# Kernel optimization log

Hardware: AMD Instinct MI355X
Metric: run time of the kernel (lower is better)

The kernel has to match this reference:

```python
import jax, jax.numpy as jnp
import numpy as np

N_NODES = 50000
N_EDGES = 600000
IN_CH = 128
HID_CH = 128
OUT_CH = 16
N_GRAPHS = 512


def gcn_conv(x, edge_index, W, b, n_nodes):
    """PyG GCNConv: add self-loops, symmetric deg normalization, linear, scatter-add."""
    src = edge_index[0]
    dst = edge_index[1]
    loop = jnp.arange(n_nodes, dtype=edge_index.dtype)
    src = jnp.concatenate([src, loop])  # [E+N]
    dst = jnp.concatenate([dst, loop])
    ones = jnp.ones(src.shape[0], dtype=x.dtype)
    deg = jax.ops.segment_sum(ones, dst, num_segments=n_nodes)  # in-degree incl. self-loop
    dinv = jnp.where(deg > 0, jax.lax.rsqrt(deg), 0.0)
    norm = dinv[src] * dinv[dst]  # [E+N]
    h = x @ W  # [N, out] linear-then-propagate, as in PyG GCNConv
    msg = h[src] * norm[:, None]  # gather + scale
    out = jax.ops.segment_sum(msg, dst, num_segments=n_nodes)
    return out + b


def global_mean_pool(x, batch, num_graphs):
    sums = jax.ops.segment_sum(x, batch, num_segments=num_graphs)
    cnt = jax.ops.segment_sum(jnp.ones(x.shape[0], dtype=x.dtype), batch, num_segments=num_graphs)
    return sums / jnp.maximum(cnt, 1.0)[:, None]


def setup_inputs() -> dict:
    key = jax.random.key(0)
    ks = jax.random.split(key, 8)
    x = jax.random.normal(ks[0], (N_NODES, IN_CH), dtype=jnp.float32)
    edge_index = jax.random.randint(ks[1], (2, N_EDGES), 0, N_NODES, dtype=jnp.int64 if jax.config.jax_enable_x64 else jnp.int32)
    batch = jnp.sort(jax.random.randint(ks[2], (N_NODES,), 0, N_GRAPHS, dtype=edge_index.dtype))
    s1 = 1.0 / np.sqrt(IN_CH)
    s2 = 1.0 / np.sqrt(HID_CH)
    W1 = jax.random.uniform(ks[3], (IN_CH, HID_CH), jnp.float32, -s1, s1)
    b1 = jnp.zeros((HID_CH,), jnp.float32)
    W2 = jax.random.uniform(ks[4], (HID_CH, HID_CH), jnp.float32, -s2, s2)
    b2 = jnp.zeros((HID_CH,), jnp.float32)
    Wfc = jax.random.uniform(ks[5], (HID_CH, OUT_CH), jnp.float32, -s2, s2)
    bfc = jax.random.uniform(ks[6], (OUT_CH,), jnp.float32, -s2, s2)
    return {"x": x, "edge_index": edge_index, "batch": batch,
            "W1": W1, "b1": b1, "W2": W2, "b2": b2, "Wfc": Wfc, "bfc": bfc}


def reference(x, edge_index, batch, W1, b1, W2, b2, Wfc, bfc):
    n = x.shape[0]
    h = jax.nn.relu(gcn_conv(x, edge_index, W1, b1, n))
    # dropout is identity in eval mode (training=False)
    h = jax.nn.relu(gcn_conv(h, edge_index, W2, b2, n))
    g = global_mean_pool(h, batch, N_GRAPHS)  # [G, hidden]
    out = jax.nn.sigmoid(g @ Wfc + bfc)  # [G, out]
    return out
```

## Files before the change

### kernel.cpp

```cpp
#include <hip/hip_runtime.h>
#include <hip/hip_fp16.h>
#include <math.h>

#define NN 50000
#define CH 128
#define NG 512
#define OCH 16
#define CAP 64
#define NBINS 196
#define HB 147

typedef _Float16 half8 __attribute__((ext_vector_type(8)));
typedef float f32x4 __attribute__((ext_vector_type(4)));
typedef float f32x2 __attribute__((ext_vector_type(2)));


__device__ __forceinline__ void unpack_fp8x8(uint2 v, float* o) {
    f32x2 a = __builtin_amdgcn_cvt_pk_f32_fp8((int)v.x, false);
    f32x2 b = __builtin_amdgcn_cvt_pk_f32_fp8((int)v.x, true);
    f32x2 c = __builtin_amdgcn_cvt_pk_f32_fp8((int)v.y, false);
    f32x2 d = __builtin_amdgcn_cvt_pk_f32_fp8((int)v.y, true);
    o[0] = a[0]; o[1] = a[1]; o[2] = b[0]; o[3] = b[1];
    o[4] = c[0]; o[5] = c[1]; o[6] = d[0]; o[7] = d[1];
}

__device__ __forceinline__ unsigned char f32_to_fp8(float v) {
    int r = __builtin_amdgcn_cvt_pk_fp8_f32(v, v, 0, false);
    return (unsigned char)(r & 0xFF);
}


__device__ __forceinline__ void gemm1_body(const float* __restrict__ A, const _Float16* __restrict__ Wt,
                                           unsigned char* __restrict__ C, int n, int blk) {
    int wave = threadIdx.x >> 6;
    int lane = threadIdx.x & 63;
    int base = blk * 64 + wave * 16;
    if (base >= n) return;
    int ma = lane & 15;
    int kb = lane >> 4;

    f32x4 acc[8];
#pragma unroll
    for (int t = 0; t < 8; ++t) acc[t] = (f32x4){0.f, 0.f, 0.f, 0.f};

#pragma unroll
    for (int kk = 0; kk < 4; ++kk) {
        int k0 = kk * 32 + kb * 8;
        const float* ap = A + (size_t)(base + ma) * CH + k0;
        float4 a0 = ((const float4*)ap)[0];
        float4 a1 = ((const float4*)ap)[1];
        half8 af;
        af[0] = (_Float16)a0.x; af[1] = (_Float16)a0.y; af[2] = (_Float16)a0.z; af[3] = (_Float16)a0.w;
        af[4] = (_Float16)a1.x; af[5] = (_Float16)a1.y; af[6] = (_Float16)a1.z; af[7] = (_Float16)a1.w;
#pragma unroll
        for (int tn = 0; tn < 8; ++tn) {
            half8 bf = *(const half8*)(Wt + (size_t)(tn * 16 + ma) * CH + k0);
            acc[tn] = __builtin_amdgcn_mfma_f32_16x16x32_f16(af, bf, acc[tn], 0, 0, 0);
        }
    }

    int r0 = base + kb * 4;
#pragma unroll
    for (int tn = 0; tn < 8; ++tn) {
#pragma unroll
        for (int r = 0; r < 4; ++r) {
            C[(size_t)(r0 + r) * CH + tn * 16 + ma] = f32_to_fp8(acc[tn][r]);
        }
    }
}


__global__ __launch_bounds__(256) void k1_hist_init_gemm1_k(const int* __restrict__ dst, int e, int* __restrict__ tableT,
                                                            const int* __restrict__ batch, int n, int* __restrict__ gstart,
                                                            const float* __restrict__ W1, const float* __restrict__ W2,
                                                            _Float16* __restrict__ Wt1, _Float16* __restrict__ Wt2,
                                                            const float* __restrict__ x, unsigned char* __restrict__ h1,
                                                            int* __restrict__ tickets) {
    if ((int)blockIdx.x < HB) {
        __shared__ int hist[NBINS];
        for (int i = threadIdx.x; i < NBINS; i += 256) hist[i] = 0;
        __syncthreads();
#pragma unroll
        for (int j = 0; j < 4; ++j) {
            int idx = blockIdx.x * 4096 + j * 1024 + threadIdx.x * 4;
            if (idx + 3 < e) {
                int4 d = *(const int4*)&dst[idx];
                atomicAdd(&hist[d.x >> 8], 1);
                atomicAdd(&hist[d.y >> 8], 1);
                atomicAdd(&hist[d.z >> 8], 1);
                atomicAdd(&hist[d.w >> 8], 1);
            } else {
                for (int k = idx; k < e && k < idx + 4; ++k) atomicAdd(&hist[dst[k] >> 8], 1);
            }
        }
        __syncthreads();
        for (int i = threadIdx.x; i < NBINS; i += 256) tableT[i * HB + blockIdx.x] = hist[i];
    } else if ((int)blockIdx.x < HB + 66) {
        int i = ((int)blockIdx.x - HB) * 256 + threadIdx.x;
        if (i < 2) tickets[i] = 0;
        if (i <= NG) {
            int lo = 0, hi = n;
            while (lo < hi) {
                int mid = (lo + hi) >> 1;
                if (batch[mid] < i) lo = mid + 1; else hi = mid;
            }
            gstart[i] = lo;
        }
        if (i < CH * CH) {
            int k = i >> 7, c = i & 127;
            Wt1[c * CH + k] = (_Float16)W1[i];
            Wt2[c * CH + k] = (_Float16)W2[i];
        }
    } else {
        gemm1_body(x, Wt1, h1, n, blockIdx.x - (HB + 66));
    }
}


__global__ __launch_bounds__(256) void scanAB_k(int* __restrict__ tableT, int* __restrict__ binsum,
                                                int* __restrict__ bin_start, int* __restrict__ ticket) {
    int w = threadIdx.x >> 6, lane = threadIdx.x & 63;
    int bin = blockIdx.x * 4 + w;
    {
        int* row = tableT + bin * HB;
        int b3 = lane * 3;
        int v0 = (b3     < HB) ? row[b3]     : 0;
        int v1 = (b3 + 1 < HB) ? row[b3 + 1] : 0;
        int v2 = (b3 + 2 < HB) ? row[b3 + 2] : 0;
        int s = v0 + v1 + v2;
        int x = s;
#pragma unroll
        for (int off = 1; off < 64; off <<= 1) {
            int y = __shfl_up(x, off);
            if (lane >= off) x += y;
        }
        int excl = x - s;
        if (b3     < HB) row[b3]     = excl;
        if (b3 + 1 < HB) row[b3 + 1] = excl + v0;
        if (b3 + 2 < HB) row[b3 + 2] = excl + v0 + v1;
        if (lane == 63) binsum[bin] = x;
    }
    __syncthreads();
    __threadfence();
    __shared__ int lastBlk;
    if (threadIdx.x == 0) lastBlk = (atomicAdd(ticket, 1) == (int)gridDim.x - 1) ? 1 : 0;
    __syncthreads();
    if (lastBlk) {
        __threadfence();
        __shared__ int s[256];
        int t = threadIdx.x;
        int v = (t < NBINS) ? binsum[t] : 0;
        s[t] = v;
        __syncthreads();
        for (int off = 1; off < 256; off <<= 1) {
            int u = (t >= off) ? s[t - off] : 0;
            __syncthreads();
            s[t] += u;
            __syncthreads();
        }
        if (t < NBINS) bin_start[t] = s[t] - v;
        if (t == NBINS - 1) bin_start[NBINS] = s[t];
    }
}


__global__ __launch_bounds__(256) void scatter_k(const int* __restrict__ src, const int* __restrict__ dst, int e,
                                                 const int* __restrict__ tableT, const int* __restrict__ bin_start,
                                                 unsigned int* __restrict__ binned) {
    __shared__ int cur[NBINS];
    for (int i = threadIdx.x; i < NBINS; i += 256) cur[i] = bin_start[i] + tableT[i * HB + blockIdx.x];
    __syncthreads();
#pragma unroll
    for (int j = 0; j < 4; ++j) {
        int idx = blockIdx.x * 4096 + j * 1024 + threadIdx.x * 4;
        if (idx + 3 < e) {
            int4 d = *(const int4*)&dst[idx];
            int4 s = *(const int4*)&src[idx];
            int p0 = atomicAdd(&cur[d.x >> 8], 1);
            int p1 = atomicAdd(&cur[d.y >> 8], 1);
            int p2 = atomicAdd(&cur[d.z >> 8], 1);
            int p3 = atomicAdd(&cur[d.w >> 8], 1);
            binned[p0] = (unsigned)s.x | ((unsigned)(d.x & 255) << 16);
            binned[p1] = (unsigned)s.y | ((unsigned)(d.y & 255) << 16);
            binned[p2] = (unsigned)s.z | ((unsigned)(d.z & 255) << 16);
            binned[p3] = (unsigned)s.w | ((unsigned)(d.w & 255) << 16);
        } else {
            for (int k = idx; k < e && k < idx + 4; ++k) {
                int d = dst[k];
                int p = atomicAdd(&cur[d >> 8], 1);
                binned[p] = (unsigned)src[k] | ((unsigned)(d & 255) << 16);
            }
        }
    }
}


__global__ __launch_bounds__(256) void bucket_k(const unsigned int* __restrict__ binned,
                                                const int* __restrict__ bin_start,
                                                int* __restrict__ cursor, int* __restrict__ csr, int n) {
    __shared__ int cur2[256];
    cur2[threadIdx.x] = 0;
    __syncthreads();
    int lo = bin_start[blockIdx.x], hi = bin_start[blockIdx.x + 1];
    for (int i = lo + threadIdx.x; i < hi; i += 256) {
        unsigned int p = binned[i];
        int local = p >> 16;
        int node = ((int)blockIdx.x << 8) | local;
        int pos = atomicAdd(&cur2[local], 1);
        if (pos < CAP) csr[(size_t)node * CAP + pos] = (int)(p & 0xFFFFu);
    }
    __syncthreads();
    int node = blockIdx.x * 256 + threadIdx.x;
    if (node < n) cursor[node] = cur2[threadIdx.x];
}


__global__ __launch_bounds__(256) void agg1_gemm2_k(const unsigned char* __restrict__ h1,
                                                    const int* __restrict__ cursor, const int* __restrict__ csr,
                                                    const float* __restrict__ b1, const _Float16* __restrict__ Wt2,
                                                    unsigned char* __restrict__ h2, int n) {
    __shared__ _Float16 xs[16][136];
    int local = threadIdx.x >> 4;
    int node = blockIdx.x * 16 + local;
    int lane = threadIdx.x & 15;
    const uint2* H = (const uint2*)h1;

    int deg = cursor[node];
    float dv = rsqrtf((float)deg + 1.0f);
    int degc = deg > CAP ? CAP : deg;

    float acc[8];
    {
        float t[8];
        unpack_fp8x8(H[(size_t)node * 16 + lane], t);
#pragma unroll
        for (int j = 0; j < 8; ++j) acc[j] = t[j] * dv;
    }
    const int4* row4 = (const int4*)(csr + (size_t)node * CAP);
    int i = 0;
    for (; i + 8 <= degc; i += 8) {
        int4 sa = row4[i >> 2];
        int4 sb = row4[(i >> 2) + 1];
        uint2 v0 = H[(size_t)sa.x * 16 + lane];
        uint2 v1 = H[(size_t)sa.y * 16 + lane];
        uint2 v2 = H[(size_t)sa.z * 16 + lane];
        uint2 v3 = H[(size_t)sa.w * 16 + lane];
        uint2 v4 = H[(size_t)sb.x * 16 + lane];
        uint2 v5 = H[(size_t)sb.y * 16 + lane];
        uint2 v6 = H[(size_t)sb.z * 16 + lane];
        uint2 v7 = H[(size_t)sb.w * 16 + lane];
        float w0 = rsqrtf((float)cursor[sa.x] + 1.0f);
        float w1 = rsqrtf((float)cursor[sa.y] + 1.0f);
        float w2 = rsqrtf((float)cursor[sa.z] + 1.0f);
        float w3 = rsqrtf((float)cursor[sa.w] + 1.0f);
        float w4 = rsqrtf((float)cursor[sb.x] + 1.0f);
        float w5 = rsqrtf((float)cursor[sb.y] + 1.0f);
        float w6 = rsqrtf((float)cursor[sb.z] + 1.0f);
        float w7 = rsqrtf((float)cursor[sb.w] + 1.0f);
        float t0[8], t1[8], t2[8], t3[8];
        unpack_fp8x8(v0, t0); unpack_fp8x8(v1, t1); unpack_fp8x8(v2, t2); unpack_fp8x8(v3, t3);
#pragma unroll
        for (int j = 0; j < 8; ++j) {
            acc[j] = fmaf(t0[j], w0, acc[j]);
            acc[j] = fmaf(t1[j], w1, acc[j]);
            acc[j] = fmaf(t2[j], w2, acc[j]);
            acc[j] = fmaf(t3[j], w3, acc[j]);
        }
        unpack_fp8x8(v4, t0); unpack_fp8x8(v5, t1); unpack_fp8x8(v6, t2); unpack_fp8x8(v7, t3);
#pragma unroll
        for (int j = 0; j < 8; ++j) {
            acc[j] = fmaf(t0[j], w4, acc[j]);
            acc[j] = fmaf(t1[j], w5, acc[j]);
            acc[j] = fmaf(t2[j], w6, acc[j]);
            acc[j] = fmaf(t3[j], w7, acc[j]);
        }
    }
    for (; i + 4 <= degc; i += 4) {
        int4 s4 = row4[i >> 2];
        uint2 v0 = H[(size_t)s4.x * 16 + lane];
        uint2 v1 = H[(size_t)s4.y * 16 + lane];
        uint2 v2 = H[(size_t)s4.z * 16 + lane];
        uint2 v3 = H[(size_t)s4.w * 16 + lane];
        float w0 = rsqrtf((float)cursor[s4.x] + 1.0f);
        float w1 = rsqrtf((float)cursor[s4.y] + 1.0f);
        float w2 = rsqrtf((float)cursor[s4.z] + 1.0f);
        float w3 = rsqrtf((float)cursor[s4.w] + 1.0f);
        float t0[8], t1[8], t2[8], t3[8];
        unpack_fp8x8(v0, t0); unpack_fp8x8(v1, t1); unpack_fp8x8(v2, t2); unpack_fp8x8(v3, t3);
#pragma unroll
        for (int j = 0; j < 8; ++j) {
            acc[j] = fmaf(t0[j], w0, acc[j]);
            acc[j] = fmaf(t1[j], w1, acc[j]);
            acc[j] = fmaf(t2[j], w2, acc[j]);
            acc[j] = fmaf(t3[j], w3, acc[j]);
        }
    }
    for (; i < degc; ++i) {
        int s = csr[(size_t)node * CAP + i];
        float w = rsqrtf((float)cursor[s] + 1.0f);
        float t[8];
        unpack_fp8x8(H[(size_t)s * 16 + lane], t);
#pragma unroll
        for (int j = 0; j < 8; ++j) acc[j] = fmaf(t[j], w, acc[j]);
    }

    float4 bb0 = ((const float4*)b1)[2 * lane];
    float4 bb1 = ((const float4*)b1)[2 * lane + 1];
    float rr[8];
    rr[0] = fmaxf(fmaf(acc[0], dv, bb0.x), 0.f);
    rr[1] = fmaxf(fmaf(acc[1], dv, bb0.y), 0.f);
    rr[2] = fmaxf(fmaf(acc[2], dv, bb0.z), 0.f);
    rr[3] = fmaxf(fmaf(acc[3], dv, bb0.w), 0.f);
    rr[4] = fmaxf(fmaf(acc[4], dv, bb1.x), 0.f);
    rr[5] = fmaxf(fmaf(acc[5], dv, bb1.y), 0.f);
    rr[6] = fmaxf(fmaf(acc[6], dv, bb1.z), 0.f);
    rr[7] = fmaxf(fmaf(acc[7], dv, bb1.w), 0.f);
    half8 hv;
#pragma unroll
    for (int j = 0; j < 8; ++j) hv[j] = (_Float16)rr[j];
    *(half8*)&xs[local][lane * 8] = hv;
    __syncthreads();

    int wave = threadIdx.x >> 6;
    int l = threadIdx.x & 63;
    int ma = l & 15;
    int kb = l >> 4;
    f32x4 acc2[2];
    acc2[0] = (f32x4){0.f, 0.f, 0.f, 0.f};
    acc2[1] = (f32x4){0.f, 0.f, 0.f, 0.f};
#pragma unroll
    for (int kk = 0; kk < 4; ++kk) {
        int k0 = kk * 32 + kb * 8;
        half8 af = *(const half8*)&xs[ma][k0];
#pragma unroll
        for (int t = 0; t < 2; ++t) {
            int tn = wave * 2 + t;
            half8 bf = *(const half8*)(Wt2 + (size_t)(tn * 16 + ma) * CH + k0);
            acc2[t] = __builtin_amdgcn_mfma_f32_16x16x32_f16(af, bf, acc2[t], 0, 0, 0);
        }
    }
    int gr0 = blockIdx.x * 16 + kb * 4;
    float dv2[4];
#pragma unroll
    for (int r = 0; r < 4; ++r) dv2[r] = rsqrtf((float)cursor[gr0 + r] + 1.0f);
#pragma unroll
    for (int t = 0; t < 2; ++t) {
        int tn = wave * 2 + t;
#pragma unroll
        for (int r = 0; r < 4; ++r) {
            h2[(size_t)(gr0 + r) * CH + tn * 16 + ma] = f32_to_fp8(acc2[t][r] * dv2[r]);
        }
    }
}


__global__ __launch_bounds__(1024) void agg2_pool_fc_k(const unsigned char* __restrict__ h2,
                                                       const int* __restrict__ cursor, const int* __restrict__ csr,
                                                       const float* __restrict__ b2, const int* __restrict__ gstart,
                                                       const float* __restrict__ Wfc, const float* __restrict__ bfc,
                                                       float* __restrict__ out) {
    __shared__ float psum[64][128];
    __shared__ float psum2[8][128];
    int g = blockIdx.x;
    int group = threadIdx.x >> 4;
    int lane = threadIdx.x & 15;
    int beg = gstart[g], end = gstart[g + 1];
    int c = end - beg;
    const uint2* H = (const uint2*)h2;

    float4 bb0 = ((const float4*)b2)[2 * lane];
    float4 bb1 = ((const float4*)b2)[2 * lane + 1];
    float bias[8] = {bb0.x, bb0.y, bb0.z, bb0.w, bb1.x, bb1.y, bb1.z, bb1.w};

    float racc[8] = {0.f, 0.f, 0.f, 0.f, 0.f, 0.f, 0.f, 0.f};

    for (int node = beg + group; node < end; node += 64) {
        int deg = cursor[node];
        float dv = rsqrtf((float)deg + 1.0f);
        int degc = deg > CAP ? CAP : deg;

        float acc[8];
        unpack_fp8x8(H[(size_t)node * 16 + lane], acc);

        const int4* row4 = (const int4*)(csr + (size_t)node * CAP);
        int i = 0;
        for (; i + 8 <= degc; i += 8) {
            int4 sa = row4[i >> 2];
            int4 sb = row4[(i >> 2) + 1];
            uint2 v0 = H[(size_t)sa.x * 16 + lane];
            uint2 v1 = H[(size_t)sa.y * 16 + lane];
            uint2 v2 = H[(size_t)sa.z * 16 + lane];
            uint2 v3 = H[(size_t)sa.w * 16 + lane];
            uint2 v4 = H[(size_t)sb.x * 16 + lane];
            uint2 v5 = H[(size_t)sb.y * 16 + lane];
            uint2 v6 = H[(size_t)sb.z * 16 + lane];
            uint2 v7 = H[(size_t)sb.w * 16 + lane];
            float t0[8], t1[8], t2[8], t3[8];
            unpack_fp8x8(v0, t0); unpack_fp8x8(v1, t1); unpack_fp8x8(v2, t2); unpack_fp8x8(v3, t3);
#pragma unroll
            for (int j = 0; j < 8; ++j) acc[j] += (t0[j] + t1[j]) + (t2[j] + t3[j]);
            unpack_fp8x8(v4, t0); unpack_fp8x8(v5, t1); unpack_fp8x8(v6, t2); unpack_fp8x8(v7, t3);
#pragma unroll
            for (int j = 0; j < 8; ++j) acc[j] += (t0[j] + t1[j]) + (t2[j] + t3[j]);
        }
        for (; i + 4 <= degc; i += 4) {
            int4 s4 = row4[i >> 2];
            uint2 v0 = H[(size_t)s4.x * 16 + lane];
            uint2 v1 = H[(size_t)s4.y * 16 + lane];
            uint2 v2 = H[(size_t)s4.z * 16 + lane];
            uint2 v3 = H[(size_t)s4.w * 16 + lane];
            float t0[8], t1[8], t2[8], t3[8];
            unpack_fp8x8(v0, t0); unpack_fp8x8(v1, t1); unpack_fp8x8(v2, t2); unpack_fp8x8(v3, t3);
#pragma unroll
            for (int j = 0; j < 8; ++j) acc[j] += (t0[j] + t1[j]) + (t2[j] + t3[j]);
        }
        for (; i < degc; ++i) {
            int s = csr[(size_t)node * CAP + i];
            float t[8];
            unpack_fp8x8(H[(size_t)s * 16 + lane], t);
#pragma unroll
            for (int j = 0; j < 8; ++j) acc[j] += t[j];
        }

#pragma unroll
        for (int j = 0; j < 8; ++j) racc[j] += fmaxf(fmaf(acc[j], dv, bias[j]), 0.f);
    }

#pragma unroll
    for (int j = 0; j < 8; ++j) psum[group][lane * 8 + j] = racc[j];
    __syncthreads();

    {
        int ch = threadIdx.x & 127;
        int seg = threadIdx.x >> 7;
        float s = 0.f;
#pragma unroll
        for (int gg = seg * 8; gg < seg * 8 + 8; ++gg) s += psum[gg][ch];
        psum2[seg][ch] = s;
    }
    __syncthreads();
    int t = threadIdx.x;
    if (t < CH) {
        float s = 0.f;
#pragma unroll
        for (int ss = 0; ss < 8; ++ss) s += psum2[ss][t];
        psum2[0][t] = s / fmaxf((float)c, 1.0f);
    }
    __syncthreads();
    if (t < OCH) {
        float acc = bfc[t];
#pragma unroll 8
        for (int k = 0; k < CH; ++k) acc = fmaf(psum2[0][k], Wfc[k * OCH + t], acc);
        out[(size_t)g * OCH + t] = 1.0f / (1.0f + expf(-acc));
    }
}

extern "C" void kernel_launch(void* const* d_in, const int* in_sizes, int n_in,
                              void* d_out, int out_size, void* d_ws, size_t ws_size,
                              hipStream_t stream) {
    const float* x    = (const float*)d_in[0];
    const int*   edge = (const int*)d_in[1];
    const int*   batch= (const int*)d_in[2];
    const float* W1   = (const float*)d_in[3];
    const float* b1   = (const float*)d_in[4];
    const float* W2   = (const float*)d_in[5];
    const float* b2   = (const float*)d_in[6];
    const float* Wfc  = (const float*)d_in[7];
    const float* bfc  = (const float*)d_in[8];
    float* out = (float*)d_out;

    const int N = NN;
    const int E = in_sizes[1] / 2;
    const int* src = edge;
    const int* dst = edge + E;

    unsigned char* h1 = (unsigned char*)d_ws;
    unsigned char* h2 = h1 + (size_t)N * CH;
    _Float16* Wt1     = (_Float16*)(h2 + (size_t)N * CH);
    _Float16* Wt2     = Wt1 + CH * CH;
    int* cursor       = (int*)(Wt2 + CH * CH);
    int* gstart       = cursor + N;
    int* csr          = gstart + NG + 4;
    int* tableT       = csr + (size_t)N * CAP;
    int* binsum       = tableT + NBINS * HB;
    int* bin_start    = binsum + 256;
    int* tickets      = bin_start + 208;
    unsigned int* binned = (unsigned int*)(tickets + 16);

    const int G = (N + 63) / 64;

    k1_hist_init_gemm1_k<<<HB + 66 + G, 256, 0, stream>>>(dst, E, tableT, batch, N, gstart,
                                                          W1, W2, Wt1, Wt2, x, h1, tickets);
    scanAB_k<<<49, 256, 0, stream>>>(tableT, binsum, bin_start, &tickets[0]);
    scatter_k<<<HB, 256, 0, stream>>>(src, dst, E, tableT, bin_start, binned);
    bucket_k<<<NBINS, 256, 0, stream>>>(binned, bin_start, cursor, csr, N);
    agg1_gemm2_k<<<N / 16, 256, 0, stream>>>(h1, cursor, csr, b1, Wt2, h2, N);
    agg2_pool_fc_k<<<NG, 1024, 0, stream>>>(h2, cursor, csr, b2, gstart, Wfc, bfc, out);
}
```

Before: 109.0 us.

## Widen gather loads to 16-byte vectors and process 32 nodes per block

Both aggregation kernels now assign 8 lanes per node, each loading a uint4 (16 fp8 channels) instead of 16 lanes loading uint2. This halves the number of gather load instructions and doubles the nodes handled per wave. agg1_gemm2 now handles 32 nodes per block, running a 2x2 MFMA tile per wave so each Wt2 fragment is reused across two row tiles, and it adds bounds checks for the tail. The 8-wide unrolled gather loop is dropped, and the pooling kernel's shared partial-sum buffer grows to 128 rows, which costs more registers and LDS per block and may lower occupancy.

```diff
diff --git a/kernel.cpp b/kernel.cpp
--- a/kernel.cpp
+++ b/kernel.cpp
@@ -15,13 +15,18 @@
 typedef float f32x2 __attribute__((ext_vector_type(2)));
 
 
-__device__ __forceinline__ void unpack_fp8x8(uint2 v, float* o) {
-    f32x2 a = __builtin_amdgcn_cvt_pk_f32_fp8((int)v.x, false);
-    f32x2 b = __builtin_amdgcn_cvt_pk_f32_fp8((int)v.x, true);
-    f32x2 c = __builtin_amdgcn_cvt_pk_f32_fp8((int)v.y, false);
-    f32x2 d = __builtin_amdgcn_cvt_pk_f32_fp8((int)v.y, true);
+__device__ __forceinline__ void unpack_fp8x8(unsigned a0, unsigned a1, float* o) {
+    f32x2 a = __builtin_amdgcn_cvt_pk_f32_fp8((int)a0, false);
+    f32x2 b = __builtin_amdgcn_cvt_pk_f32_fp8((int)a0, true);
+    f32x2 c = __builtin_amdgcn_cvt_pk_f32_fp8((int)a1, false);
+    f32x2 d = __builtin_amdgcn_cvt_pk_f32_fp8((int)a1, true);
     o[0] = a[0]; o[1] = a[1]; o[2] = b[0]; o[3] = b[1];
     o[4] = c[0]; o[5] = c[1]; o[6] = d[0]; o[7] = d[1];
+}
+
+__device__ __forceinline__ void unpack_fp8x16(uint4 v, float* o) {
+    unpack_fp8x8(v.x, v.y, o);
+    unpack_fp8x8(v.z, v.w, o + 8);
 }
 
 __device__ __forceinline__ unsigned char f32_to_fp8(float v) {
@@ -219,136 +224,114 @@
                                                     const int* __restrict__ cursor, const int* __restrict__ csr,
                                                     const float* __restrict__ b1, const _Float16* __restrict__ Wt2,
                                                     unsigned char* __restrict__ h2, int n) {
-    __shared__ _Float16 xs[16][136];
-    int local = threadIdx.x >> 4;
-    int node = blockIdx.x * 16 + local;
-    int lane = threadIdx.x & 15;
-    const uint2* H = (const uint2*)h1;
-
-    int deg = cursor[node];
-    float dv = rsqrtf((float)deg + 1.0f);
-    int degc = deg > CAP ? CAP : deg;
-
-    float acc[8];
-    {
-        float t[8];
-        unpack_fp8x8(H[(size_t)node * 16 + lane], t);
-#pragma unroll
-        for (int j = 0; j < 8; ++j) acc[j] = t[j] * dv;
-    }
-    const int4* row4 = (const int4*)(csr + (size_t)node * CAP);
-    int i = 0;
-    for (; i + 8 <= degc; i += 8) {
-        int4 sa = row4[i >> 2];
-        int4 sb = row4[(i >> 2) + 1];
-        uint2 v0 = H[(size_t)sa.x * 16 + lane];
-        uint2 v1 = H[(size_t)sa.y * 16 + lane];
-        uint2 v2 = H[(size_t)sa.z * 16 + lane];
-        uint2 v3 = H[(size_t)sa.w * 16 + lane];
-        uint2 v4 = H[(size_t)sb.x * 16 + lane];
-        uint2 v5 = H[(size_t)sb.y * 16 + lane];
-        uint2 v6 = H[(size_t)sb.z * 16 + lane];
-        uint2 v7 = H[(size_t)sb.w * 16 + lane];
-        float w0 = rsqrtf((float)cursor[sa.x] + 1.0f);
-        float w1 = rsqrtf((float)cursor[sa.y] + 1.0f);
-        float w2 = rsqrtf((float)cursor[sa.z] + 1.0f);
-        float w3 = rsqrtf((float)cursor[sa.w] + 1.0f);
-        float w4 = rsqrtf((float)cursor[sb.x] + 1.0f);
-        float w5 = rsqrtf((float)cursor[sb.y] + 1.0f);
-        float w6 = rsqrtf((float)cursor[sb.z] + 1.0f);
-        float w7 = rsqrtf((float)cursor[sb.w] + 1.0f);
-        float t0[8], t1[8], t2[8], t3[8];
-        unpack_fp8x8(v0, t0); unpack_fp8x8(v1, t1); unpack_fp8x8(v2, t2); unpack_fp8x8(v3, t3);
-#pragma unroll
-        for (int j = 0; j < 8; ++j) {
-            acc[j] = fmaf(t0[j], w0, acc[j]);
-            acc[j] = fmaf(t1[j], w1, acc[j]);
-            acc[j] = fmaf(t2[j], w2, acc[j]);
-            acc[j] = fmaf(t3[j], w3, acc[j]);
-        }
-        unpack_fp8x8(v4, t0); unpack_fp8x8(v5, t1); unpack_fp8x8(v6, t2); unpack_fp8x8(v7, t3);
-#pragma unroll
-        for (int j = 0; j < 8; ++j) {
-            acc[j] = fmaf(t0[j], w4, acc[j]);
-            acc[j] = fmaf(t1[j], w5, acc[j]);
-            acc[j] = fmaf(t2[j], w6, acc[j]);
-            acc[j] = fmaf(t3[j], w7, acc[j]);
-        }
-    }
-    for (; i + 4 <= degc; i += 4) {
-        int4 s4 = row4[i >> 2];
-        uint2 v0 = H[(size_t)s4.x * 16 + lane];
-        uint2 v1 = H[(size_t)s4.y * 16 + lane];
-        uint2 v2 = H[(size_t)s4.z * 16 + lane];
-        uint2 v3 = H[(size_t)s4.w * 16 + lane];
-        float w0 = rsqrtf((float)cursor[s4.x] + 1.0f);
-        float w1 = rsqrtf((float)cursor[s4.y] + 1.0f);
-        float w2 = rsqrtf((float)cursor[s4.z] + 1.0f);
-        float w3 = rsqrtf((float)cursor[s4.w] + 1.0f);
-        float t0[8], t1[8], t2[8], t3[8];
-        unpack_fp8x8(v0, t0); unpack_fp8x8(v1, t1); unpack_fp8x8(v2, t2); unpack_fp8x8(v3, t3);
-#pragma unroll
-        for (int j = 0; j < 8; ++j) {
-            acc[j] = fmaf(t0[j], w0, acc[j]);
-            acc[j] = fmaf(t1[j], w1, acc[j]);
-            acc[j] = fmaf(t2[j], w2, acc[j]);
-            acc[j] = fmaf(t3[j], w3, acc[j]);
-        }
-    }
-    for (; i < degc; ++i) {
-        int s = csr[(size_t)node * CAP + i];
-        float w = rsqrtf((float)cursor[s] + 1.0f);
-        float t[8];
-        unpack_fp8x8(H[(size_t)s * 16 + lane], t);
-#pragma unroll
-        for (int j = 0; j < 8; ++j) acc[j] = fmaf(t[j], w, acc[j]);
-    }
-
-    float4 bb0 = ((const float4*)b1)[2 * lane];
-    float4 bb1 = ((const float4*)b1)[2 * lane + 1];
-    float rr[8];
-    rr[0] = fmaxf(fmaf(acc[0], dv, bb0.x), 0.f);
-    rr[1] = fmaxf(fmaf(acc[1], dv, bb0.y), 0.f);
-    rr[2] = fmaxf(fmaf(acc[2], dv, bb0.z), 0.f);
-    rr[3] = fmaxf(fmaf(acc[3], dv, bb0.w), 0.f);
-    rr[4] = fmaxf(fmaf(acc[4], dv, bb1.x), 0.f);
-    rr[5] = fmaxf(fmaf(acc[5], dv, bb1.y), 0.f);
-    rr[6] = fmaxf(fmaf(acc[6], dv, bb1.z), 0.f);
-    rr[7] = fmaxf(fmaf(acc[7], dv, bb1.w), 0.f);
-    half8 hv;
-#pragma unroll
-    for (int j = 0; j < 8; ++j) hv[j] = (_Float16)rr[j];
-    *(half8*)&xs[local][lane * 8] = hv;
+    __shared__ _Float16 xs[32][136];
+    int local = threadIdx.x >> 3;
+    int node = blockIdx.x * 32 + local;
+    int lane = threadIdx.x & 7;
+    const uint4* H = (const uint4*)h1;
+
+    if (node < n) {
+        int deg = cursor[node];
+        float dv = rsqrtf((float)deg + 1.0f);
+        int degc = deg > CAP ? CAP : deg;
+
+        float acc[16];
+        {
+            float t[16];
+            unpack_fp8x16(H[(size_t)node * 8 + lane], t);
+#pragma unroll
+            for (int j = 0; j < 16; ++j) acc[j] = t[j] * dv;
+        }
+        const int4* row4 = (const int4*)(csr + (size_t)node * CAP);
+        int i = 0;
+        for (; i + 4 <= degc; i += 4) {
+            int4 s4 = row4[i >> 2];
+            uint4 v0 = H[(size_t)s4.x * 8 + lane];
+            uint4 v1 = H[(size_t)s4.y * 8 + lane];
+            uint4 v2 = H[(size_t)s4.z * 8 + lane];
+            uint4 v3 = H[(size_t)s4.w * 8 + lane];
+            float w0 = rsqrtf((float)cursor[s4.x] + 1.0f);
+            float w1 = rsqrtf((float)cursor[s4.y] + 1.0f);
+            float w2 = rsqrtf((float)cursor[s4.z] + 1.0f);
+            float w3 = rsqrtf((float)cursor[s4.w] + 1.0f);
+            float t0[16], t1[16], t2[16], t3[16];
+            unpack_fp8x16(v0, t0); unpack_fp8x16(v1, t1);
+            unpack_fp8x16(v2, t2); unpack_fp8x16(v3, t3);
+#pragma unroll
+            for (int j = 0; j < 16; ++j) {
+                acc[j] = fmaf(t0[j], w0, acc[j]);
+                acc[j] = fmaf(t1[j], w1, acc[j]);
+                acc[j] = fmaf(t2[j], w2, acc[j]);
+                acc[j] = fmaf(t3[j], w3, acc[j]);
+            }
+        }
+        for (; i < degc; ++i) {
+            int s = csr[(size_t)node * CAP + i];
+            float w = rsqrtf((float)cursor[s] + 1.0f);
+            float t[16];
+            unpack_fp8x16(H[(size_t)s * 8 + lane], t);
+#pragma unroll
+            for (int j = 0; j < 16; ++j) acc[j] = fmaf(t[j], w, acc[j]);
+        }
+
+        half8 hv0, hv1;
+#pragma unroll
+        for (int q = 0; q < 4; ++q) {
+            float4 bb = ((const float4*)b1)[4 * lane + q];
+            float r0 = fmaxf(fmaf(acc[4 * q + 0], dv, bb.x), 0.f);
+            float r1 = fmaxf(fmaf(acc[4 * q + 1], dv, bb.y), 0.f);
+            float r2 = fmaxf(fmaf(acc[4 * q + 2], dv, bb.z), 0.f);
+            float r3 = fmaxf(fmaf(acc[4 * q + 3], dv, bb.w), 0.f);
+            if (q < 2) {
+                hv0[4 * q + 0] = (_Float16)r0; hv0[4 * q + 1] = (_Float16)r1;
+                hv0[4 * q + 2] = (_Float16)r2; hv0[4 * q + 3] = (_Float16)r3;
+            } else {
+                hv1[4 * (q - 2) + 0] = (_Float16)r0; hv1[4 * (q - 2) + 1] = (_Float16)r1;
+                hv1[4 * (q - 2) + 2] = (_Float16)r2; hv1[4 * (q - 2) + 3] = (_Float16)r3;
+            }
+        }
+        ((half8*)&xs[local][lane * 16])[0] = hv0;
+        ((half8*)&xs[local][lane * 16])[1] = hv1;
+    } else {
+        half8 z = (half8){0, 0, 0, 0, 0, 0, 0, 0};
+        ((half8*)&xs[local][lane * 16])[0] = z;
+        ((half8*)&xs[local][lane * 16])[1] = z;
+    }
     __syncthreads();
 
     int wave = threadIdx.x >> 6;
     int l = threadIdx.x & 63;
     int ma = l & 15;
     int kb = l >> 4;
-    f32x4 acc2[2];
-    acc2[0] = (f32x4){0.f, 0.f, 0.f, 0.f};
-    acc2[1] = (f32x4){0.f, 0.f, 0.f, 0.f};
+    f32x4 acc00 = (f32x4){0.f, 0.f, 0.f, 0.f}, acc01 = acc00, acc10 = acc00, acc11 = acc00;
 #pragma unroll
     for (int kk = 0; kk < 4; ++kk) {
         int k0 = kk * 32 + kb * 8;
-        half8 af = *(const half8*)&xs[ma][k0];
-#pragma unroll
-        for (int t = 0; t < 2; ++t) {
-            int tn = wave * 2 + t;
-            half8 bf = *(const half8*)(Wt2 + (size_t)(tn * 16 + ma) * CH + k0);
-            acc2[t] = __builtin_amdgcn_mfma_f32_16x16x32_f16(af, bf, acc2[t], 0, 0, 0);
-        }
-    }
-    int gr0 = blockIdx.x * 16 + kb * 4;
-    float dv2[4];
-#pragma unroll
-    for (int r = 0; r < 4; ++r) dv2[r] = rsqrtf((float)cursor[gr0 + r] + 1.0f);
-#pragma unroll
-    for (int t = 0; t < 2; ++t) {
-        int tn = wave * 2 + t;
-#pragma unroll
-        for (int r = 0; r < 4; ++r) {
-            h2[(size_t)(gr0 + r) * CH + tn * 16 + ma] = f32_to_fp8(acc2[t][r] * dv2[r]);
+        half8 af0 = *(const half8*)&xs[ma][k0];
+        half8 af1 = *(const half8*)&xs[16 + ma][k0];
+        half8 bf0 = *(const half8*)(Wt2 + (size_t)((wave * 2 + 0) * 16 + ma) * CH + k0);
+        half8 bf1 = *(const half8*)(Wt2 + (size_t)((wave * 2 + 1) * 16 + ma) * CH + k0);
+        acc00 = __builtin_amdgcn_mfma_f32_16x16x32_f16(af0, bf0, acc00, 0, 0, 0);
+        acc01 = __builtin_amdgcn_mfma_f32_16x16x32_f16(af0, bf1, acc01, 0, 0, 0);
+        acc10 = __builtin_amdgcn_mfma_f32_16x16x32_f16(af1, bf0, acc10, 0, 0, 0);
+        acc11 = __builtin_amdgcn_mfma_f32_16x16x32_f16(af1, bf1, acc11, 0, 0, 0);
+    }
+    int base = blockIdx.x * 32;
+#pragma unroll
+    for (int rt = 0; rt < 2; ++rt) {
+        int gr0 = base + rt * 16 + kb * 4;
+        float dv2[4];
+#pragma unroll
+        for (int r = 0; r < 4; ++r) dv2[r] = (gr0 + r < n) ? rsqrtf((float)cursor[gr0 + r] + 1.0f) : 0.f;
+#pragma unroll
+        for (int ct = 0; ct < 2; ++ct) {
+            int tn = wave * 2 + ct;
+            f32x4 a = (rt == 0) ? (ct == 0 ? acc00 : acc01) : (ct == 0 ? acc10 : acc11);
+#pragma unroll
+            for (int r = 0; r < 4; ++r) {
+                if (gr0 + r < n)
+                    h2[(size_t)(gr0 + r) * CH + tn * 16 + ma] = f32_to_fp8(a[r] * dv2[r]);
+            }
         }
     }
 }
@@ -359,75 +342,68 @@
                                                        const float* __restrict__ b2, const int* __restrict__ gstart,
                                                        const float* __restrict__ Wfc, const float* __restrict__ bfc,
                                                        float* __restrict__ out) {
-    __shared__ float psum[64][128];
+    __shared__ float psum[128][128];
     __shared__ float psum2[8][128];
     int g = blockIdx.x;
-    int group = threadIdx.x >> 4;
-    int lane = threadIdx.x & 15;
+    int group = threadIdx.x >> 3;
+    int lane = threadIdx.x & 7;
     int beg = gstart[g], end = gstart[g + 1];
     int c = end - beg;
-    const uint2* H = (const uint2*)h2;
-
-    float4 bb0 = ((const float4*)b2)[2 * lane];
-    float4 bb1 = ((const float4*)b2)[2 * lane + 1];
-    float bias[8] = {bb0.x, bb0.y, bb0.z, bb0.w, bb1.x, bb1.y, bb1.z, bb1.w};
-
-    float racc[8] = {0.f, 0.f, 0.f, 0.f, 0.f, 0.f, 0.f, 0.f};
-
-    for (int node = beg + group; node < end; node += 64) {
+    const uint4* H = (const uint4*)h2;
+
+    float bias[16];
+#pragma unroll
+    for (int q = 0; q < 4; ++q) {
+        float4 bb = ((const float4*)b2)[4 * lane + q];
+        bias[4 * q + 0] = bb.x; bias[4 * q + 1] = bb.y;
+        bias[4 * q + 2] = bb.z; bias[4 * q + 3] = bb.w;
+    }
+
+    float racc[16];
+#pragma unroll
+    for (int j = 0; j < 16; ++j) racc[j] = 0.f;
+
+    for (int node = beg + group; node < end; node += 128) {
         int deg = cursor[node];
         float dv = rsqrtf((float)deg + 1.0f);
         int degc = deg > CAP ? CAP : deg;
 
-        float acc[8];
-        unpack_fp8x8(H[(size_t)node * 16 + lane], acc);
+        float acc[16];
+        unpack_fp8x16(H[(size_t)node * 8 + lane], acc);
 
         const int4* row4 = (const int4*)(csr + (size_t)node * CAP);
         int i = 0;
-        for (; i + 8 <= degc; i += 8) {
-            int4 sa = row4[i >> 2];
-            int4 sb = row4[(i >> 2) + 1];
-            uint2 v0 = H[(size_t)sa.x * 16 + lane];
-            uint2 v1 = H[(size_t)sa.y * 16 + lane];
-            uint2 v2 = H[(size_t)sa.z * 16 + lane];
-            uint2 v3 = H[(size_t)sa.w * 16 + lane];
-            uint2 v4 = H[(size_t)sb.x * 16 + lane];
-            uint2 v5 = H[(size_t)sb.y * 16 + lane];
-            uint2 v6 = H[(size_t)sb.z * 16 + lane];
-            uint2 v7 = H[(size_t)sb.w * 16 + lane];
-            float t0[8], t1[8], t2[8], t3[8];
-            unpack_fp8x8(v0, t0); unpack_fp8x8(v1, t1); unpack_fp8x8(v2, t2); unpack_fp8x8(v3, t3);
-#pragma unroll
-            for (int j = 0; j < 8; ++j) acc[j] += (t0[j] + t1[j]) + (t2[j] + t3[j]);
-            unpack_fp8x8(v4, t0); unpack_fp8x8(v5, t1); unpack_fp8x8(v6, t2); unpack_fp8x8(v7, t3);
-#pragma unroll
-            for (int j = 0; j < 8; ++j) acc[j] += (t0[j] + t1[j]) + (t2[j] + t3[j]);
-        }
         for (; i + 4 <= degc; i += 4) {
             int4 s4 = row4[i >> 2];
-            uint2 v0 = H[(size_t)s4.x * 16 + lane];
-            uint2 v1 = H[(size_t)s4.y * 16 + lane];
-            uint2 v2 = H[(size_t)s4.z * 16 + lane];
-            uint2 v3 = H[(size_t)s4.w * 16 + lane];
-            float t0[8], t1[8], t2[8], t3[8];
-            unpack_fp8x8(v0, t0); unpack_fp8x8(v1, t1); unpack_fp8x8(v2, t2); unpack_fp8x8(v3, t3);
-#pragma unroll
-            for (int j = 0; j < 8; ++j) acc[j] += (t0[j] + t1[j]) + (t2[j] + t3[j]);
+            uint4 v0 = H[(size_t)s4.x * 8 + lane];
+            uint4 v1 = H[(size_t)s4.y * 8 + lane];
+            uint4 v2 = H[(size_t)s4.z * 8 + lane];
+            uint4 v3 = H[(size_t)s4.w * 8 + lane];
+            float t0[16], t1[16], t2[16], t3[16];
+            unpack_fp8x16(v0, t0); unpack_fp8x16(v1, t1);
+            unpack_fp8x16(v2, t2); unpack_fp8x16(v3, t3);
+#pragma unroll
+            for (int j = 0; j < 16; ++j) acc[j] += (t0[j] + t1[j]) + (t2[j] + t3[j]);
         }
         for (; i < degc; ++i) {
             int s = csr[(size_t)node * CAP + i];
-            float t[8];
-            unpack_fp8x8(H[(size_t)s * 16 + lane], t);
-#pragma unroll
-            for (int j = 0; j < 8; ++j) acc[j] += t[j];
-        }
-
-#pragma unroll
-        for (int j = 0; j < 8; ++j) racc[j] += fmaxf(fmaf(acc[j], dv, bias[j]), 0.f);
-    }
-
-#pragma unroll
-    for (int j = 0; j < 8; ++j) psum[group][lane * 8 + j] = racc[j];
+            float t[16];
+            unpack_fp8x16(H[(size_t)s * 8 + lane], t);
+#pragma unroll
+            for (int j = 0; j < 16; ++j) acc[j] += t[j];
+        }
+
+#pragma unroll
+        for (int j = 0; j < 16; ++j) racc[j] += fmaxf(fmaf(acc[j], dv, bias[j]), 0.f);
+    }
+
+#pragma unroll
+    for (int q = 0; q < 4; ++q) {
+        float4 v;
+        v.x = racc[4 * q + 0]; v.y = racc[4 * q + 1];
+        v.z = racc[4 * q + 2]; v.w = racc[4 * q + 3];
+        ((float4*)&psum[group][lane * 16])[q] = v;
+    }
     __syncthreads();
 
     {
@@ -435,7 +411,7 @@
         int seg = threadIdx.x >> 7;
         float s = 0.f;
 #pragma unroll
-        for (int gg = seg * 8; gg < seg * 8 + 8; ++gg) s += psum[gg][ch];
+        for (int gg = seg * 16; gg < seg * 16 + 16; ++gg) s += psum[gg][ch];
         psum2[seg][ch] = s;
     }
     __syncthreads();
@@ -494,6 +470,6 @@
     scanAB_k<<<49, 256, 0, stream>>>(tableT, binsum, bin_start, &tickets[0]);
     scatter_k<<<HB, 256, 0, stream>>>(src, dst, E, tableT, bin_start, binned);
     bucket_k<<<NBINS, 256, 0, stream>>>(binned, bin_start, cursor, csr, N);
-    agg1_gemm2_k<<<N / 16, 256, 0, stream>>>(h1, cursor, csr, b1, Wt2, h2, N);
+    agg1_gemm2_k<<<(N + 31) / 32, 256, 0, stream>>>(h1, cursor, csr, b1, Wt2, h2, N);
     agg2_pool_fc_k<<<NG, 1024, 0, stream>>>(h2, cursor, csr, b2, gstart, Wfc, bfc, out);
 }
```

After: 105.5 us. -3.2%, faster.
